# Kernel tuning notes

Hardware: AMD Instinct MI355X
Metric: run time of the kernel (lower is better)

## Reference

```python
import jax, jax.numpy as jnp
import numpy as np

EMBED = 1024
B, S = 4, 2048


def setup_inputs() -> dict:
    key = jax.random.key(0)
    ks = jax.random.split(key, 10)
    scale = 1.0 / np.sqrt(EMBED)
    return {
        "query": jax.random.normal(ks[0], (B, S, EMBED), jnp.float32),
        "key": jax.random.normal(ks[1], (B, S, EMBED), jnp.float32),
        "value": jax.random.normal(ks[2], (B, S, EMBED), jnp.float32),
        "attn_mask": jnp.zeros((B, S, S), jnp.float32),
        "Wq": jax.random.normal(ks[3], (EMBED, EMBED), jnp.float32) * scale,
        "bq": jnp.zeros((EMBED,), jnp.float32),
        "Wk": jax.random.normal(ks[4], (EMBED, EMBED), jnp.float32) * scale,
        "bk": jnp.zeros((EMBED,), jnp.float32),
        "Wv": jax.random.normal(ks[5], (EMBED, EMBED), jnp.float32) * scale,
        "bv": jnp.zeros((EMBED,), jnp.float32),
    }


def reference(query, key, value, attn_mask, Wq, bq, Wk, bk, Wv, bv):
    # Linear projections (torch Linear: x @ W.T + b)
    q = jnp.einsum("bse,fe->bsf", query, Wq) + bq
    k = jnp.einsum("bse,fe->bsf", key, Wk) + bk
    v = jnp.einsum("bse,fe->bsf", value, Wv) + bv
    # Scaled dot-product attention; NOTE: scale is sqrt(embed_size) (full dim),
    # matching the original module exactly (num_heads is unused there).
    inv_scale = 1.0 / jnp.sqrt(jnp.asarray(q.shape[-1], q.dtype))
    qk = jnp.einsum("bqe,bke->bqk", q, k) * inv_scale + attn_mask
    attn = jax.nn.softmax(qk, axis=-1)
    # dropout_p = 0.0 (eval-mode identity)
    return jnp.einsum("bqk,bke->bqe", attn, v)
```

## Files before the change

kernel.cpp:

```cpp
#include <hip/hip_runtime.h>
#include <stdint.h>


typedef __attribute__((ext_vector_type(8))) short s8v;
typedef __attribute__((ext_vector_type(4))) float f32x4;

__device__ __forceinline__ unsigned short f2b(float f) {
  union { float f; unsigned u; } c; c.f = f;
  unsigned r = c.u + 0x7fffu + ((c.u >> 16) & 1u);
  return (unsigned short)(r >> 16);
}
__device__ __forceinline__ float b2f(unsigned short s) {
  union { float f; unsigned u; } c; c.u = ((unsigned)s) << 16; return c.f;
}

__device__ __forceinline__ void gload_lds16(const void* gsrc, void* ldst) {
  __builtin_amdgcn_global_load_lds(
      (__attribute__((address_space(1))) unsigned int*)(uintptr_t)gsrc,
      (__attribute__((address_space(3))) unsigned int*)(unsigned)(uintptr_t)ldst,
      16, 0, 0);
}

template <bool OUT_BF16, int BIAS, bool MASK>
__global__ __launch_bounds__(256, 2) void gemm_nt(
    const unsigned short* __restrict__ A, long strideAb, int lda,
    const unsigned short* __restrict__ B, long strideBb, int ldb,
    void* __restrict__ Cptr, long strideCb, int ldc,
    const float* __restrict__ bias,
    const float* __restrict__ maskp, long strideMb, int ldM,
    int M, int N, int K, float scale, int tilesN) {
  __shared__ __align__(16) short AsS[128 * 64];
  __shared__ __align__(16) short BsS[128 * 64];

  const int tid = threadIdx.x;
  const int lane = tid & 63;
  const int w = tid >> 6;
  const int wr = w >> 1, wc = w & 1;
  const int batch = blockIdx.y;
  const int tm = blockIdx.x / tilesN, tn = blockIdx.x % tilesN;
  const int brow = tm * 128, bcol = tn * 128;

  const unsigned short* aSrc = A + (long)batch * strideAb +
      (long)(brow + w * 32 + (lane >> 3)) * lda + (lane & 7) * 8;
  const unsigned short* bSrc = B + (long)batch * strideBb +
      (long)(bcol + w * 32 + (lane >> 3)) * ldb + (lane & 7) * 8;

  f32x4 acc[4][4];
#pragma unroll
  for (int i = 0; i < 4; i++)
#pragma unroll
    for (int j = 0; j < 4; j++) acc[i][j] = (f32x4){0.f, 0.f, 0.f, 0.f};

  const int fr = lane & 15;
  const int fq = lane >> 4;
  const int nk = K >> 6;

  for (int kt = 0; kt < nk; kt++) {
#pragma unroll
    for (int i = 0; i < 4; i++) {
      gload_lds16(aSrc + (long)i * 8 * lda, &AsS[w * 2048 + i * 512]);
      gload_lds16(bSrc + (long)i * 8 * ldb, &BsS[w * 2048 + i * 512]);
    }
    aSrc += 64; bSrc += 64;
    __syncthreads();
#pragma unroll
    for (int ks = 0; ks < 2; ks++) {
      s8v af[4], bf[4];
#pragma unroll
      for (int mi = 0; mi < 4; mi++)
        af[mi] = *(const s8v*)&AsS[(wr * 64 + mi * 16 + fr) * 64 + ks * 32 + fq * 8];
#pragma unroll
      for (int ni = 0; ni < 4; ni++)
        bf[ni] = *(const s8v*)&BsS[(wc * 64 + ni * 16 + fr) * 64 + ks * 32 + fq * 8];
#pragma unroll
      for (int mi = 0; mi < 4; mi++)
#pragma unroll
        for (int ni = 0; ni < 4; ni++)
          acc[mi][ni] = __builtin_amdgcn_mfma_f32_16x16x32_bf16(
              af[mi], bf[ni], acc[mi][ni], 0, 0, 0);
    }
    __syncthreads();
  }

  unsigned short* Cb = (unsigned short*)Cptr;
  float* Cf = (float*)Cptr;
  const long cB = (long)batch * strideCb;
  const float* maskB = MASK ? (maskp + (long)batch * strideMb) : nullptr;
#pragma unroll
  for (int mi = 0; mi < 4; mi++) {
#pragma unroll
    for (int ni = 0; ni < 4; ni++) {
      const int col = bcol + wc * 64 + ni * 16 + fr;
#pragma unroll
      for (int r = 0; r < 4; r++) {
        const int row = brow + wr * 64 + mi * 16 + fq * 4 + r;
        float v = acc[mi][ni][r] * scale;
        if (BIAS == 1) v += bias[col];
        if (BIAS == 2) v += bias[row];
        if (MASK) v += maskB[(long)row * ldM + col];
        if (OUT_BF16) Cb[cB + (long)row * ldc + col] = f2b(v);
        else          Cf[cB + (long)row * ldc + col] = v;
      }
    }
  }
}

__global__ __launch_bounds__(256) void cvt_f32_bf16(
    const float* __restrict__ in, unsigned short* __restrict__ out, long n8) {
  long i = (long)blockIdx.x * blockDim.x + threadIdx.x;
  const long stride = (long)gridDim.x * blockDim.x;
  for (; i < n8; i += stride) {
    const float* p = in + i * 8;
    f32x4 a = *(const f32x4*)p;
    f32x4 b = *(const f32x4*)(p + 4);
    s8v o;
    o[0] = (short)f2b(a[0]); o[1] = (short)f2b(a[1]);
    o[2] = (short)f2b(a[2]); o[3] = (short)f2b(a[3]);
    o[4] = (short)f2b(b[0]); o[5] = (short)f2b(b[1]);
    o[6] = (short)f2b(b[2]); o[7] = (short)f2b(b[3]);
    *(s8v*)(out + i * 8) = o;
  }
}

__global__ __launch_bounds__(256) void softmax_inplace(unsigned short* __restrict__ S) {
  const long row = blockIdx.x;
  unsigned short* rp = S + row * 2048;
  const int tid = threadIdx.x, lane = tid & 63, wid = tid >> 6;

  s8v vb = *(const s8v*)&rp[tid * 8];
  float x[8];
#pragma unroll
  for (int j = 0; j < 8; j++) x[j] = b2f((unsigned short)vb[j]);

  float m = x[0];
#pragma unroll
  for (int j = 1; j < 8; j++) m = fmaxf(m, x[j]);
#pragma unroll
  for (int off = 32; off > 0; off >>= 1) m = fmaxf(m, __shfl_xor(m, off, 64));

  __shared__ float red[4];
  if (lane == 0) red[wid] = m;
  __syncthreads();
  m = fmaxf(fmaxf(red[0], red[1]), fmaxf(red[2], red[3]));
  __syncthreads();

  float s = 0.f;
#pragma unroll
  for (int j = 0; j < 8; j++) { x[j] = __expf(x[j] - m); s += x[j]; }
#pragma unroll
  for (int off = 32; off > 0; off >>= 1) s += __shfl_xor(s, off, 64);
  if (lane == 0) red[wid] = s;
  __syncthreads();
  s = red[0] + red[1] + red[2] + red[3];
  const float inv = 1.0f / s;

  s8v ob;
#pragma unroll
  for (int j = 0; j < 8; j++) ob[j] = (short)f2b(x[j] * inv);
  *(s8v*)&rp[tid * 8] = ob;
}

extern "C" void kernel_launch(void* const* d_in, const int* in_sizes, int n_in,
                              void* d_out, int out_size, void* d_ws, size_t ws_size,
                              hipStream_t stream) {
  const float* q    = (const float*)d_in[0];
  const float* k    = (const float*)d_in[1];
  const float* v    = (const float*)d_in[2];
  const float* mask = (const float*)d_in[3];
  const float* Wq   = (const float*)d_in[4];
  const float* bq   = (const float*)d_in[5];
  const float* Wk   = (const float*)d_in[6];
  const float* bk   = (const float*)d_in[7];
  const float* Wv   = (const float*)d_in[8];
  const float* bv   = (const float*)d_in[9];
  float* out = (float*)d_out;

  const size_t MB = 1ull << 20;
  if (ws_size < 134 * MB) return;
  char* ws = (char*)d_ws;
  unsigned short* qb  = (unsigned short*)(ws + 0 * MB);
  unsigned short* kb  = (unsigned short*)(ws + 16 * MB);
  unsigned short* vT  = (unsigned short*)(ws + 32 * MB);
  unsigned short* Sb  = (unsigned short*)(ws + 48 * MB);
  unsigned short* xq  = (unsigned short*)(ws + 80 * MB);
  unsigned short* xk  = (unsigned short*)(ws + 96 * MB);
  unsigned short* xv  = (unsigned short*)(ws + 112 * MB);
  unsigned short* Wqb = (unsigned short*)(ws + 128 * MB);
  unsigned short* Wkb = (unsigned short*)(ws + 130 * MB);
  unsigned short* Wvb = (unsigned short*)(ws + 132 * MB);

  const long NX = 4L * 2048 * 1024;
  const long NW = 1024L * 1024;

  cvt_f32_bf16<<<2048, 256, 0, stream>>>(q, xq, NX / 8);
  cvt_f32_bf16<<<2048, 256, 0, stream>>>(k, xk, NX / 8);
  cvt_f32_bf16<<<2048, 256, 0, stream>>>(v, xv, NX / 8);
  cvt_f32_bf16<<<512, 256, 0, stream>>>(Wq, Wqb, NW / 8);
  cvt_f32_bf16<<<512, 256, 0, stream>>>(Wk, Wkb, NW / 8);
  cvt_f32_bf16<<<512, 256, 0, stream>>>(Wv, Wvb, NW / 8);

  gemm_nt<true, 1, false><<<dim3(64 * 8, 1), 256, 0, stream>>>(
      xq, 0, 1024, Wqb, 0, 1024, (void*)qb, 0, 1024,
      bq, nullptr, 0, 0, 8192, 1024, 1024, 1.0f, 8);
  gemm_nt<true, 1, false><<<dim3(64 * 8, 1), 256, 0, stream>>>(
      xk, 0, 1024, Wkb, 0, 1024, (void*)kb, 0, 1024,
      bk, nullptr, 0, 0, 8192, 1024, 1024, 1.0f, 8);
  gemm_nt<true, 2, false><<<dim3(8 * 16, 4), 256, 0, stream>>>(
      Wvb, 0, 1024, xv, 2048L * 1024, 1024, (void*)vT, 1024L * 2048, 2048,
      bv, nullptr, 0, 0, 1024, 2048, 1024, 1.0f, 16);
  gemm_nt<true, 0, true><<<dim3(16 * 16, 4), 256, 0, stream>>>(
      qb, 2048L * 1024, 1024, kb, 2048L * 1024, 1024, (void*)Sb, 2048L * 2048, 2048,
      nullptr, mask, 2048L * 2048, 2048, 2048, 2048, 1024, 0.03125f, 16);
  softmax_inplace<<<8192, 256, 0, stream>>>(Sb);
  gemm_nt<false, 0, false><<<dim3(16 * 8, 4), 256, 0, stream>>>(
      Sb, 2048L * 2048, 2048, vT, 1024L * 2048, 2048, (void*)out, 2048L * 1024, 1024,
      nullptr, nullptr, 0, 0, 2048, 1024, 2048, 1.0f, 8);
}
```

Measured before the change: 261.5 us.

## Replace GEMMs with 256x256 double-buffered 8-wave pipelined kernel, batch launches

```diff
diff --git a/kernel.cpp b/kernel.cpp
--- a/kernel.cpp
+++ b/kernel.cpp
@@ -21,104 +21,232 @@
       16, 0, 0);
 }
 
-template <bool OUT_BF16, int BIAS, bool MASK>
-__global__ __launch_bounds__(256, 2) void gemm_nt(
-    const unsigned short* __restrict__ A, long strideAb, int lda,
-    const unsigned short* __restrict__ B, long strideBb, int ldb,
-    void* __restrict__ Cptr, long strideCb, int ldc,
-    const float* __restrict__ bias,
-    const float* __restrict__ maskp, long strideMb, int ldM,
-    int M, int N, int K, float scale, int tilesN) {
-  __shared__ __align__(16) short AsS[128 * 64];
-  __shared__ __align__(16) short BsS[128 * 64];
+template <int N> __device__ __forceinline__ void waitvm() {
+  if constexpr (N == 4)      asm volatile("s_waitcnt vmcnt(4)" ::: "memory");
+  else if constexpr (N == 2) asm volatile("s_waitcnt vmcnt(2)" ::: "memory");
+  else                       asm volatile("s_waitcnt vmcnt(0)" ::: "memory");
+}
+#define BAR() do { __builtin_amdgcn_sched_barrier(0); \
+  asm volatile("s_barrier" ::: "memory"); \
+  __builtin_amdgcn_sched_barrier(0); } while (0)
+
+struct Job {
+  const unsigned short* A; const unsigned short* B; void* C;
+  const float* bias; const float* mask;
+  long sAb, sBb, sCb, sMb;
+  int lda, ldb, ldc, ldM;
+  int K, tilesN, tilesMN;
+  float scale; int flags;
+};
+
+__global__ __launch_bounds__(512, 2) void gemm8p(Job j0, Job j1, Job j2,
+                                                 int b0, int b1) {
+  __shared__ __align__(16) char lds[131072];
+
+  const int nwg = gridDim.x;
+  int hw = blockIdx.x;
+  int g = (hw & 7) * (nwg >> 3) + (hw >> 3);
+  const Job J = (g < b0) ? j0 : (g < b1) ? j1 : j2;
+  g -= (g < b0) ? 0 : (g < b1) ? b0 : b1;
+
+  const int batch = g / J.tilesMN;
+  const int tt = g - batch * J.tilesMN;
+  const int tm = tt / J.tilesN, tn = tt - tm * J.tilesN;
+  const int brow = tm << 8, bcol = tn << 8;
 
   const int tid = threadIdx.x;
-  const int lane = tid & 63;
-  const int w = tid >> 6;
-  const int wr = w >> 1, wc = w & 1;
-  const int batch = blockIdx.y;
-  const int tm = blockIdx.x / tilesN, tn = blockIdx.x % tilesN;
-  const int brow = tm * 128, bcol = tn * 128;
-
-  const unsigned short* aSrc = A + (long)batch * strideAb +
-      (long)(brow + w * 32 + (lane >> 3)) * lda + (lane & 7) * 8;
-  const unsigned short* bSrc = B + (long)batch * strideBb +
-      (long)(bcol + w * 32 + (lane >> 3)) * ldb + (lane & 7) * 8;
-
-  f32x4 acc[4][4];
-#pragma unroll
-  for (int i = 0; i < 4; i++)
-#pragma unroll
-    for (int j = 0; j < 4; j++) acc[i][j] = (f32x4){0.f, 0.f, 0.f, 0.f};
-
-  const int fr = lane & 15;
-  const int fq = lane >> 4;
-  const int nk = K >> 6;
-
-  for (int kt = 0; kt < nk; kt++) {
-#pragma unroll
-    for (int i = 0; i < 4; i++) {
-      gload_lds16(aSrc + (long)i * 8 * lda, &AsS[w * 2048 + i * 512]);
-      gload_lds16(bSrc + (long)i * 8 * ldb, &BsS[w * 2048 + i * 512]);
-    }
-    aSrc += 64; bSrc += 64;
-    __syncthreads();
-#pragma unroll
-    for (int ks = 0; ks < 2; ks++) {
-      s8v af[4], bf[4];
-#pragma unroll
-      for (int mi = 0; mi < 4; mi++)
-        af[mi] = *(const s8v*)&AsS[(wr * 64 + mi * 16 + fr) * 64 + ks * 32 + fq * 8];
-#pragma unroll
-      for (int ni = 0; ni < 4; ni++)
-        bf[ni] = *(const s8v*)&BsS[(wc * 64 + ni * 16 + fr) * 64 + ks * 32 + fq * 8];
-#pragma unroll
-      for (int mi = 0; mi < 4; mi++)
-#pragma unroll
-        for (int ni = 0; ni < 4; ni++)
+  const int lane = tid & 63, w = tid >> 6;
+  const int wm = w >> 2, wn = w & 3;
+  const int fr = lane & 15, fq = lane >> 4;
+
+  const unsigned short* Ab = J.A + (long)batch * J.sAb;
+  const unsigned short* Bb = J.B + (long)batch * J.sBb;
+
+  const unsigned short* srcA[2][2]; const unsigned short* srcB[2][2];
+  int dstO[2][2];
+#pragma unroll
+  for (int h = 0; h < 2; h++)
+#pragma unroll
+    for (int i = 0; i < 2; i++) {
+      const int P = h * 16384 + w * 2048 + i * 1024 + lane * 16;
+      const int L = P ^ (((P >> 9) & 3) << 5);
+      const int row = L >> 7, colb = L & 127;
+      srcA[h][i] = Ab + (long)(brow + row) * J.lda + (colb >> 1);
+      srcB[h][i] = Bb + (long)(bcol + row) * J.ldb + (colb >> 1);
+      dstO[h][i] = h * 16384 + w * 2048 + i * 1024;
+    }
+
+  int offA[8], offB[4];
+#pragma unroll
+  for (int mi = 0; mi < 8; mi++) {
+    const int rowL = (mi < 4 ? wm * 64 + mi * 16 : 128 + wm * 64 + (mi - 4) * 16) + fr;
+    offA[mi] = (rowL * 128 + fq * 16) ^ (((rowL >> 2) & 3) << 5);
+  }
+#pragma unroll
+  for (int ni = 0; ni < 4; ni++) {
+    const int rowL = (ni < 2 ? wn * 32 + ni * 16 : 128 + wn * 32 + (ni - 2) * 16) + fr;
+    offB[ni] = (rowL * 128 + fq * 16) ^ (((rowL >> 2) & 3) << 5);
+  }
+
+  f32x4 acc[8][4];
+#pragma unroll
+  for (int mi = 0; mi < 8; mi++)
+#pragma unroll
+    for (int ni = 0; ni < 4; ni++) acc[mi][ni] = (f32x4){0.f, 0.f, 0.f, 0.f};
+
+  const int NT = J.K >> 6;
+
+#define STG_A(h, kt, d1) { \
+  gload_lds16(srcA[h][0] + (long)(kt) * 64, lds + (d1) * 32768 + dstO[h][0]); \
+  gload_lds16(srcA[h][1] + (long)(kt) * 64, lds + (d1) * 32768 + dstO[h][1]); }
+#define STG_B(h, kt, d1) { \
+  gload_lds16(srcB[h][0] + (long)(kt) * 64, lds + 65536 + (d1) * 32768 + dstO[h][0]); \
+  gload_lds16(srcB[h][1] + (long)(kt) * 64, lds + 65536 + (d1) * 32768 + dstO[h][1]); }
+
+  STG_A(0, 0, 0); STG_B(0, 0, 0); STG_B(1, 0, 0); STG_A(1, 0, 0);
+  waitvm<4>();
+  BAR();
+
+  s8v a[4][2], bb0[2][2], bb1[2][2];
+  for (int t = 0; t < NT; ++t) {
+    const int d = t & 1, d1 = d ^ 1;
+    const char* rdA = lds + d * 32768;
+    const char* rdB = lds + 65536 + d * 32768;
+    const bool st = (t + 1 < NT);
+
+#pragma unroll
+    for (int mi = 0; mi < 4; mi++) {
+      a[mi][0] = *(const s8v*)(rdA + offA[mi]);
+      a[mi][1] = *(const s8v*)(rdA + (offA[mi] ^ 64));
+    }
+#pragma unroll
+    for (int ni = 0; ni < 2; ni++) {
+      bb0[ni][0] = *(const s8v*)(rdB + offB[ni]);
+      bb0[ni][1] = *(const s8v*)(rdB + (offB[ni] ^ 64));
+    }
+    if (st) STG_A(0, t + 1, d1);
+    BAR();
+    __builtin_amdgcn_s_setprio(1);
+#pragma unroll
+    for (int mi = 0; mi < 4; mi++)
+#pragma unroll
+      for (int ni = 0; ni < 2; ni++)
+#pragma unroll
+        for (int ks = 0; ks < 2; ks++)
           acc[mi][ni] = __builtin_amdgcn_mfma_f32_16x16x32_bf16(
-              af[mi], bf[ni], acc[mi][ni], 0, 0, 0);
-    }
-    __syncthreads();
-  }
-
-  unsigned short* Cb = (unsigned short*)Cptr;
-  float* Cf = (float*)Cptr;
-  const long cB = (long)batch * strideCb;
-  const float* maskB = MASK ? (maskp + (long)batch * strideMb) : nullptr;
-#pragma unroll
-  for (int mi = 0; mi < 4; mi++) {
+              a[mi][ks], bb0[ni][ks], acc[mi][ni], 0, 0, 0);
+    __builtin_amdgcn_s_setprio(0);
+    if (st) waitvm<4>(); else waitvm<2>();
+    BAR();
+
+#pragma unroll
+    for (int ni = 0; ni < 2; ni++) {
+      bb1[ni][0] = *(const s8v*)(rdB + offB[2 + ni]);
+      bb1[ni][1] = *(const s8v*)(rdB + (offB[2 + ni] ^ 64));
+    }
+    if (st) STG_B(0, t + 1, d1);
+    BAR();
+    __builtin_amdgcn_s_setprio(1);
+#pragma unroll
+    for (int mi = 0; mi < 4; mi++)
+#pragma unroll
+      for (int ni = 0; ni < 2; ni++)
+#pragma unroll
+        for (int ks = 0; ks < 2; ks++)
+          acc[mi][2 + ni] = __builtin_amdgcn_mfma_f32_16x16x32_bf16(
+              a[mi][ks], bb1[ni][ks], acc[mi][2 + ni], 0, 0, 0);
+    __builtin_amdgcn_s_setprio(0);
+    if (st) waitvm<4>(); else waitvm<0>();
+    BAR();
+
+#pragma unroll
+    for (int mi = 0; mi < 4; mi++) {
+      a[mi][0] = *(const s8v*)(rdA + offA[4 + mi]);
+      a[mi][1] = *(const s8v*)(rdA + (offA[4 + mi] ^ 64));
+    }
+    if (st) STG_B(1, t + 1, d1);
+    BAR();
+    __builtin_amdgcn_s_setprio(1);
+#pragma unroll
+    for (int mi = 0; mi < 4; mi++)
+#pragma unroll
+      for (int ni = 0; ni < 2; ni++)
+#pragma unroll
+        for (int ks = 0; ks < 2; ks++)
+          acc[4 + mi][2 + ni] = __builtin_amdgcn_mfma_f32_16x16x32_bf16(
+              a[mi][ks], bb1[ni][ks], acc[4 + mi][2 + ni], 0, 0, 0);
+    __builtin_amdgcn_s_setprio(0);
+    BAR();
+
+    if (st) STG_A(1, t + 1, d1);
+    BAR();
+    __builtin_amdgcn_s_setprio(1);
+#pragma unroll
+    for (int mi = 0; mi < 4; mi++)
+#pragma unroll
+      for (int ni = 0; ni < 2; ni++)
+#pragma unroll
+        for (int ks = 0; ks < 2; ks++)
+          acc[4 + mi][ni] = __builtin_amdgcn_mfma_f32_16x16x32_bf16(
+              a[mi][ks], bb0[ni][ks], acc[4 + mi][ni], 0, 0, 0);
+    __builtin_amdgcn_s_setprio(0);
+    if (st) waitvm<4>();
+    BAR();
+  }
+
+  const int obf = J.flags & 1, bmode = (J.flags >> 1) & 3, hasM = (J.flags >> 3) & 1;
+  unsigned short* Cb = (unsigned short*)J.C;
+  float* Cf = (float*)J.C;
+  const long cB = (long)batch * J.sCb;
+  const float* maskB = J.mask + (long)batch * J.sMb;
+#pragma unroll
+  for (int mi = 0; mi < 8; mi++) {
+    const int rloc = (mi < 4 ? wm * 64 + mi * 16 : 128 + wm * 64 + (mi - 4) * 16) + fq * 4;
 #pragma unroll
     for (int ni = 0; ni < 4; ni++) {
-      const int col = bcol + wc * 64 + ni * 16 + fr;
+      const int col = bcol + (ni < 2 ? wn * 32 + ni * 16 : 128 + wn * 32 + (ni - 2) * 16) + fr;
 #pragma unroll
       for (int r = 0; r < 4; r++) {
-        const int row = brow + wr * 64 + mi * 16 + fq * 4 + r;
-        float v = acc[mi][ni][r] * scale;
-        if (BIAS == 1) v += bias[col];
-        if (BIAS == 2) v += bias[row];
-        if (MASK) v += maskB[(long)row * ldM + col];
-        if (OUT_BF16) Cb[cB + (long)row * ldc + col] = f2b(v);
-        else          Cf[cB + (long)row * ldc + col] = v;
+        const int row = brow + rloc + r;
+        float v = acc[mi][ni][r] * J.scale;
+        if (bmode == 1) v += J.bias[col];
+        if (bmode == 2) v += J.bias[row];
+        if (hasM) v += maskB[(long)row * J.ldM + col];
+        if (obf) Cb[cB + (long)row * J.ldc + col] = f2b(v);
+        else     Cf[cB + (long)row * J.ldc + col] = v;
       }
     }
   }
-}
-
-__global__ __launch_bounds__(256) void cvt_f32_bf16(
-    const float* __restrict__ in, unsigned short* __restrict__ out, long n8) {
-  long i = (long)blockIdx.x * blockDim.x + threadIdx.x;
-  const long stride = (long)gridDim.x * blockDim.x;
-  for (; i < n8; i += stride) {
-    const float* p = in + i * 8;
-    f32x4 a = *(const f32x4*)p;
-    f32x4 b = *(const f32x4*)(p + 4);
+#undef STG_A
+#undef STG_B
+}
+
+__global__ __launch_bounds__(256) void cvt6(
+    const float* s0, unsigned short* d0, const float* s1, unsigned short* d1,
+    const float* s2, unsigned short* d2, const float* s3, unsigned short* d3,
+    const float* s4, unsigned short* d4, const float* s5, unsigned short* d5) {
+  int bid = blockIdx.x;
+  const float* src; unsigned short* dst; long n8; int lb, nb;
+  if (bid < 2304) {
+    int r = bid / 768; lb = bid - r * 768; nb = 768; n8 = 1048576;
+    src = r == 0 ? s0 : r == 1 ? s1 : s2;
+    dst = r == 0 ? d0 : r == 1 ? d1 : d2;
+  } else {
+    int r = (bid - 2304) / 128; lb = (bid - 2304) - r * 128; nb = 128; n8 = 131072;
+    src = r == 0 ? s3 : r == 1 ? s4 : s5;
+    dst = r == 0 ? d3 : r == 1 ? d4 : d5;
+  }
+  const long stride = (long)nb * 256;
+  for (long i = (long)lb * 256 + threadIdx.x; i < n8; i += stride) {
+    const float* p = src + i * 8;
+    f32x4 va = *(const f32x4*)p;
+    f32x4 vb = *(const f32x4*)(p + 4);
     s8v o;
-    o[0] = (short)f2b(a[0]); o[1] = (short)f2b(a[1]);
-    o[2] = (short)f2b(a[2]); o[3] = (short)f2b(a[3]);
-    o[4] = (short)f2b(b[0]); o[5] = (short)f2b(b[1]);
-    o[6] = (short)f2b(b[2]); o[7] = (short)f2b(b[3]);
-    *(s8v*)(out + i * 8) = o;
+    o[0] = (short)f2b(va[0]); o[1] = (short)f2b(va[1]);
+    o[2] = (short)f2b(va[2]); o[3] = (short)f2b(va[3]);
+    o[4] = (short)f2b(vb[0]); o[5] = (short)f2b(vb[1]);
+    o[6] = (short)f2b(vb[2]); o[7] = (short)f2b(vb[3]);
+    *(s8v*)(dst + i * 8) = o;
   }
 }
 
@@ -189,30 +317,25 @@
   unsigned short* Wkb = (unsigned short*)(ws + 130 * MB);
   unsigned short* Wvb = (unsigned short*)(ws + 132 * MB);
 
-  const long NX = 4L * 2048 * 1024;
-  const long NW = 1024L * 1024;
-
-  cvt_f32_bf16<<<2048, 256, 0, stream>>>(q, xq, NX / 8);
-  cvt_f32_bf16<<<2048, 256, 0, stream>>>(k, xk, NX / 8);
-  cvt_f32_bf16<<<2048, 256, 0, stream>>>(v, xv, NX / 8);
-  cvt_f32_bf16<<<512, 256, 0, stream>>>(Wq, Wqb, NW / 8);
-  cvt_f32_bf16<<<512, 256, 0, stream>>>(Wk, Wkb, NW / 8);
-  cvt_f32_bf16<<<512, 256, 0, stream>>>(Wv, Wvb, NW / 8);
-
-  gemm_nt<true, 1, false><<<dim3(64 * 8, 1), 256, 0, stream>>>(
-      xq, 0, 1024, Wqb, 0, 1024, (void*)qb, 0, 1024,
-      bq, nullptr, 0, 0, 8192, 1024, 1024, 1.0f, 8);
-  gemm_nt<true, 1, false><<<dim3(64 * 8, 1), 256, 0, stream>>>(
-      xk, 0, 1024, Wkb, 0, 1024, (void*)kb, 0, 1024,
-      bk, nullptr, 0, 0, 8192, 1024, 1024, 1.0f, 8);
-  gemm_nt<true, 2, false><<<dim3(8 * 16, 4), 256, 0, stream>>>(
-      Wvb, 0, 1024, xv, 2048L * 1024, 1024, (void*)vT, 1024L * 2048, 2048,
-      bv, nullptr, 0, 0, 1024, 2048, 1024, 1.0f, 16);
-  gemm_nt<true, 0, true><<<dim3(16 * 16, 4), 256, 0, stream>>>(
-      qb, 2048L * 1024, 1024, kb, 2048L * 1024, 1024, (void*)Sb, 2048L * 2048, 2048,
-      nullptr, mask, 2048L * 2048, 2048, 2048, 2048, 1024, 0.03125f, 16);
+  cvt6<<<2688, 256, 0, stream>>>(q, xq, k, xk, v, xv, Wq, Wqb, Wk, Wkb, Wv, Wvb);
+
+  Job jq = { xq, Wqb, (void*)qb, bq, nullptr, 0, 0, 0, 0,
+             1024, 1024, 1024, 0, 1024, 4, 128, 1.0f, 1 | (1 << 1) };
+  Job jk = { xk, Wkb, (void*)kb, bk, nullptr, 0, 0, 0, 0,
+             1024, 1024, 1024, 0, 1024, 4, 128, 1.0f, 1 | (1 << 1) };
+  Job jv = { Wvb, xv, (void*)vT, bv, nullptr, 0, 2048L * 1024, 1024L * 2048, 0,
+             1024, 1024, 2048, 0, 1024, 8, 32, 1.0f, 1 | (2 << 1) };
+  gemm8p<<<384, 512, 0, stream>>>(jq, jk, jv, 128, 256);
+
+  Job js = { qb, kb, (void*)Sb, nullptr, mask,
+             2048L * 1024, 2048L * 1024, 2048L * 2048, 2048L * 2048,
+             1024, 1024, 2048, 2048, 1024, 8, 64, 0.03125f, 1 | (1 << 3) };
+  gemm8p<<<256, 512, 0, stream>>>(js, js, js, 256, 256);
+
   softmax_inplace<<<8192, 256, 0, stream>>>(Sb);
-  gemm_nt<false, 0, false><<<dim3(16 * 8, 4), 256, 0, stream>>>(
-      Sb, 2048L * 2048, 2048, vT, 1024L * 2048, 2048, (void*)out, 2048L * 1024, 1024,
-      nullptr, nullptr, 0, 0, 2048, 1024, 2048, 1.0f, 8);
-}
+
+  Job jp = { Sb, vT, (void*)out, nullptr, nullptr,
+             2048L * 2048, 1024L * 2048, 2048L * 1024, 0,
+             2048, 2048, 1024, 0, 2048, 4, 32, 1.0f, 0 };
+  gemm8p<<<128, 512, 0, stream>>>(jp, jp, jp, 128, 128);
+}
```

After: 328.4 us. +25.6%, slower.
